# Optimization experiments

Hardware: AMD Instinct MI355X
Metric: run time of the kernel (lower is better)

Reference implementation:

```python
import jax, jax.numpy as jnp
import numpy as np

NUM_RBF = 16
RBF_D_MIN, RBF_D_MAX = 2.0, 22.0
CB_A, CB_B, CB_C = -0.58273431, 0.56802827, -0.54067466
TOP_K = 32
MAX_REL = 32
NPOS = 16
HID = 128
LN_EPS = 1e-5


def _gather_nodes(nodes, idx):
    # nodes: (B, L, D), idx: (B, L, K) -> (B, L, K, D)
    return jax.vmap(lambda n, i: n[i])(nodes, idx)


def _rbf_encode(D):
    mu = jnp.linspace(RBF_D_MIN, RBF_D_MAX, NUM_RBF, dtype=D.dtype)
    sigma = (RBF_D_MAX - RBF_D_MIN) / NUM_RBF
    return jnp.exp(-((D[..., None] - mu) ** 2) / (sigma ** 2))


def setup_inputs() -> dict:
    key = jax.random.key(0)
    ks = jax.random.split(key, 4)
    B, L = 2, 2048
    X = jax.random.normal(ks[0], (B, L, 4, 3), jnp.float32) * 10.0
    residue_mask = jnp.ones((B, L), jnp.float32)
    R_idx = jnp.arange(B * L, dtype=jnp.int32).reshape(B, L)
    chain_labels = jnp.zeros((B, L), jnp.int32)
    # learned params
    W_pos = jax.random.normal(ks[1], (NPOS, 2 * MAX_REL + 2), jnp.float32) * 0.05
    b_pos = jnp.zeros((NPOS,), jnp.float32)
    W_edge = jax.random.normal(ks[2], (HID, 25 * NUM_RBF + NPOS), jnp.float32) * 0.02
    ln_gamma = jnp.ones((HID,), jnp.float32)
    ln_beta = jnp.zeros((HID,), jnp.float32)
    return {"X": X, "residue_mask": residue_mask, "R_idx": R_idx,
            "chain_labels": chain_labels, "W_pos": W_pos, "b_pos": b_pos,
            "W_edge": W_edge, "ln_gamma": ln_gamma, "ln_beta": ln_beta}


def reference(X, residue_mask, R_idx, chain_labels, W_pos, b_pos, W_edge, ln_gamma, ln_beta):
    B, L = X.shape[0], X.shape[1]
    K = min(TOP_K, L)
    # virtual CB from backbone N, CA, C
    N, CA, C = X[..., 0, :], X[..., 1, :], X[..., 2, :]
    b = CA - N
    c = C - CA
    a = jnp.cross(b, c, axis=-1)
    CB = (CB_A * a + CB_B * b + CB_C * c + CA)[..., None, :]
    atoms_5 = jnp.concatenate([X, CB], axis=-2)  # (B, L, 5, 3)
    # kNN on CA coords with invalid residues pushed far away
    diff = CA[:, :, None, :] - CA[:, None, :, :]
    dist_sq = jnp.sum(diff * diff, axis=-1)  # (B, L, L)
    inv_mask = 1.0 - residue_mask
    dist_sq = dist_sq + inv_mask[:, None, :] * 1e6
    _, E_idx = jax.lax.top_k(-dist_sq, K)  # smallest-k indices, (B, L, K)
    # gather neighbor 5-atom coords and compute 25 pairwise distances
    Xf = atoms_5.reshape(B, L, 15)
    Xg = _gather_nodes(Xf, E_idx).reshape(B, L, K, 5, 3)
    d2 = jnp.sum((atoms_5[:, :, None, :, None, :] - Xg[:, :, :, None, :, :]) ** 2, axis=-1)
    D = jnp.sqrt(d2 + 1e-6)  # (B, L, K, 5, 5)
    rbf = _rbf_encode(D).reshape(B, L, K, 25 * NUM_RBF)
    # positional encodings (standard ProteinMPNN form)
    Rg = _gather_nodes(R_idx[..., None], E_idx)[..., 0]  # (B, L, K)
    Cg = _gather_nodes(chain_labels[..., None], E_idx)[..., 0]
    d_rel = Rg - R_idx[:, :, None]
    same_chain = (Cg == chain_labels[:, :, None])
    d_clip = jnp.clip(d_rel + MAX_REL, 0, 2 * MAX_REL)
    d_final = jnp.where(same_chain, d_clip, 2 * MAX_REL + 1)
    oh = jax.nn.one_hot(d_final, 2 * MAX_REL + 2, dtype=rbf.dtype)
    pos_enc = jnp.einsum('blkc,pc->blkp', oh, W_pos) + b_pos
    # edge embedding + layernorm
    edge_input = jnp.concatenate([pos_enc, rbf], axis=-1)  # (B, L, K, 416)
    h = jnp.einsum('blkf,hf->blkh', edge_input, W_edge)
    mean = jnp.mean(h, axis=-1, keepdims=True)
    var = jnp.var(h, axis=-1, keepdims=True)
    E = (h - mean) * jax.lax.rsqrt(var + LN_EPS) * ln_gamma + ln_beta
    return E_idx, E
```

## Files before the change

kernel.cpp:

```cpp
#include <hip/hip_runtime.h>
#include <hip/hip_bf16.h>

#define LEN   2048
#define KNB   32
#define HID   128

typedef unsigned long long ull;
typedef unsigned int uint32;
typedef __bf16 bf16x8 __attribute__((ext_vector_type(8)));
typedef float  f32x4  __attribute__((ext_vector_type(4)));

__global__ __launch_bounds__(256) void prep_kernel(
    const float* __restrict__ X, const float* __restrict__ mask,
    const float* __restrict__ W_edge,
    float4* __restrict__ CAm, __bf16* __restrict__ Wbf) {
    const int t = blockIdx.x * 256 + threadIdx.x;
    if (t < 2 * LEN) {
        const float* p = X + (size_t)t * 12;
        CAm[t] = make_float4(p[3], p[4], p[5],
                             __fmul_rn(__fsub_rn(1.0f, mask[t]), 1000000.0f));
    }
    Wbf[t] = (__bf16)W_edge[t];
}

__global__ __launch_bounds__(256) void topk_kernel(
    const float4* __restrict__ CAm, float* __restrict__ eidx_out) {
    const int row = blockIdx.x;
    const int b = row >> 11;
    const int i = row & (LEN - 1);
    const int tid = threadIdx.x;

    __shared__ int hist[512];
    __shared__ ull cand[LEN];
    __shared__ int candcnt;
    __shared__ int selB;

    const float4* C = CAm + (size_t)b * LEN;
    const float4 ci = C[i];

    uint32 d2b[8];
#pragma unroll
    for (int q = 0; q < 8; ++q) {
        const float4 cj = C[q * 256 + tid];
        float dx = __fsub_rn(ci.x, cj.x);
        float dy = __fsub_rn(ci.y, cj.y);
        float dz = __fsub_rn(ci.z, cj.z);
        float d2 = __fadd_rn(__fadd_rn(__fmul_rn(dx, dx), __fmul_rn(dy, dy)),
                             __fmul_rn(dz, dz));
        d2 = __fadd_rn(d2, cj.w);
        d2b[q] = __float_as_uint(d2);
    }

    hist[tid] = 0; hist[tid + 256] = 0;
    if (tid == 0) candcnt = 0;
    __syncthreads();
#pragma unroll
    for (int q = 0; q < 8; ++q) atomicAdd(&hist[d2b[q] >> 22], 1);
    __syncthreads();

    if (tid < 64) {
        int loc[8];
        int s = 0;
#pragma unroll
        for (int t = 0; t < 8; ++t) { loc[t] = hist[tid * 8 + t]; s += loc[t]; }
        int incl = s;
#pragma unroll
        for (int off = 1; off < 64; off <<= 1) {
            int o = __shfl_up(incl, off, 64);
            if (tid >= off) incl += o;
        }
        const int excl = incl - s;
        if (excl < KNB && incl >= KNB) {
            int c = excl;
#pragma unroll
            for (int t = 0; t < 8; ++t) {
                int c2 = c + loc[t];
                if (c < KNB && c2 >= KNB) selB = tid * 8 + t;
                c = c2;
            }
        }
    }
    __syncthreads();
    const uint32 B = (uint32)selB;

#pragma unroll
    for (int q = 0; q < 8; ++q) {
        if ((d2b[q] >> 22) <= B) {
            int p = atomicAdd(&candcnt, 1);
            cand[p] = (((ull)d2b[q]) << 32) | (uint32)(q * 256 + tid);
        }
    }
    __syncthreads();
    const int M = candcnt;

    for (int c = tid; c < M; c += 256) {
        const ull k = cand[c];
        int r = 0;
        for (int m = 0; m < M; ++m) r += (cand[m] < k);
        if (r < KNB)
            eidx_out[(size_t)row * KNB + r] = (float)(uint32)(k & 0xFFFFFFFFull);
    }
}

__device__ __forceinline__ void load_res_atoms(const float* __restrict__ p, float* dst) {
    const float Nx = p[0], Ny = p[1], Nz = p[2];
    const float Ax = p[3], Ay = p[4], Az = p[5];
    const float Cx = p[6], Cy = p[7], Cz = p[8];
    const float Ox = p[9], Oy = p[10], Oz = p[11];
    const float bx = Ax - Nx, by = Ay - Ny, bz = Az - Nz;
    const float cx = Cx - Ax, cy = Cy - Ay, cz = Cz - Az;
    const float axv = by * cz - bz * cy;
    const float ayv = bz * cx - bx * cz;
    const float azv = bx * cy - by * cx;
    dst[0] = Nx;  dst[1] = Ny;  dst[2] = Nz;
    dst[3] = Ax;  dst[4] = Ay;  dst[5] = Az;
    dst[6] = Cx;  dst[7] = Cy;  dst[8] = Cz;
    dst[9] = Ox;  dst[10] = Oy; dst[11] = Oz;
    dst[12] = -0.58273431f * axv + 0.56802827f * bx + -0.54067466f * cx + Ax;
    dst[13] = -0.58273431f * ayv + 0.56802827f * by + -0.54067466f * cy + Ay;
    dst[14] = -0.58273431f * azv + 0.56802827f * bz + -0.54067466f * cz + Az;
}

#define FSTRIDE 424

__global__ __launch_bounds__(512, 4) void edge_kernel(
    const float* __restrict__ X,
    const int* __restrict__ Ridx, const int* __restrict__ Chain,
    const float* __restrict__ W_pos, const float* __restrict__ b_pos,
    const __bf16* __restrict__ Wbf,
    const float* __restrict__ lng, const float* __restrict__ lnb,
    const float* __restrict__ eidx_f, float* __restrict__ outE) {
    const int tid = threadIdx.x;
    const int row0 = blockIdx.x * 8;
    const int b = row0 >> 11;
    const int i0 = row0 & (LEN - 1);

    __shared__ __align__(16) __bf16 featE[32 * FSTRIDE];
    __shared__ __align__(16) float hbuf[32 * 132];
    __shared__ float natoms8[8][32][17];
    __shared__ float iatoms8[8][16];
    __shared__ int jR8[8][32], jC8[8][32];

    const float* Xb = X + (size_t)b * LEN * 12;

    const int w = tid >> 6, l = tid & 63, lr = l & 15, lg = l >> 4;
    bf16x8 wreg[13];
    {
        const __bf16* wb = Wbf + (size_t)(w * 16 + lr) * 416 + lg * 8;
#pragma unroll
        for (int ks = 0; ks < 13; ++ks)
            wreg[ks] = *(const bf16x8*)(wb + ks * 32);
    }

    if (tid < 256) {
        const int r8 = tid >> 5, e = tid & 31;
        const int j = (int)eidx_f[(size_t)(row0 + r8) * KNB + e];
        jR8[r8][e] = Ridx[b * LEN + j];
        jC8[r8][e] = Chain[b * LEN + j];
        load_res_atoms(Xb + j * 12, &natoms8[r8][e][0]);
    } else if (tid < 264) {
        const int r8 = tid - 256;
        load_res_atoms(Xb + (size_t)(i0 + r8) * 12, &iatoms8[r8][0]);
    }
    __syncthreads();

    for (int r8 = 0; r8 < 8; ++r8) {
        const int row = row0 + r8;
        const int i = i0 + r8;
        const int Ri = Ridx[b * LEN + i];
        const int Ci = Chain[b * LEN + i];

        {
            const int e = tid >> 4, p = tid & 15;
            const int drel = jR8[r8][e] - Ri;
            const int same = (jC8[r8][e] == Ci);
            int dc = drel + 32;
            dc = dc < 0 ? 0 : (dc > 64 ? 64 : dc);
            const int df = same ? dc : 65;
            featE[e * FSTRIDE + p] = (__bf16)(W_pos[p * 66 + df] + b_pos[p]);
        }
#pragma unroll
        for (int it = 0; it < 2; ++it) {
            const int task = tid + it * 512;
            if (task < 800) {
                const int mn = task >> 5, e = task & 31;
                const int m = mn / 5, n = mn - m * 5;
                const float ax = iatoms8[r8][m * 3 + 0];
                const float ay = iatoms8[r8][m * 3 + 1];
                const float az = iatoms8[r8][m * 3 + 2];
                const float* na = &natoms8[r8][e][n * 3];
                const float dx = ax - na[0], dy = ay - na[1], dz = az - na[2];
                const float D = sqrtf(dx * dx + dy * dy + dz * dz + 1e-6f);
                bf16x8 v0, v1;
#pragma unroll
                for (int r = 0; r < 8; ++r) {
                    const float mu = (float)(2.0 + (double)r * (20.0 / 15.0));
                    const float t = D - mu;
                    v0[r] = (__bf16)__expf(-(t * t) * (1.0f / 1.5625f));
                }
#pragma unroll
                for (int r = 8; r < 16; ++r) {
                    const float mu = (float)(2.0 + (double)r * (20.0 / 15.0));
                    const float t = D - mu;
                    v1[r - 8] = (__bf16)__expf(-(t * t) * (1.0f / 1.5625f));
                }
                *(bf16x8*)(featE + e * FSTRIDE + 16 + mn * 16)     = v0;
                *(bf16x8*)(featE + e * FSTRIDE + 16 + mn * 16 + 8) = v1;
            }
        }
        __syncthreads();

        f32x4 acc0 = {0.f, 0.f, 0.f, 0.f}, acc1 = acc0;
        const __bf16* fb0 = featE + lr * FSTRIDE + lg * 8;
        const __bf16* fb1 = featE + (16 + lr) * FSTRIDE + lg * 8;
#pragma unroll
        for (int ks = 0; ks < 13; ++ks) {
            const bf16x8 a0 = *(const bf16x8*)(fb0 + ks * 32);
            const bf16x8 a1 = *(const bf16x8*)(fb1 + ks * 32);
            acc0 = __builtin_amdgcn_mfma_f32_16x16x32_bf16(a0, wreg[ks], acc0, 0, 0, 0);
            acc1 = __builtin_amdgcn_mfma_f32_16x16x32_bf16(a1, wreg[ks], acc1, 0, 0, 0);
        }
#pragma unroll
        for (int rr = 0; rr < 4; ++rr) {
            hbuf[(lg * 4 + rr) * 132 + w * 16 + lr]        = acc0[rr];
            hbuf[(16 + lg * 4 + rr) * 132 + w * 16 + lr]   = acc1[rr];
        }
        __syncthreads();

        const int g = tid >> 4, l2 = tid & 15;
        const float4* hb4 = (const float4*)(hbuf + g * 132 + l2 * 8);
        const float4 v0 = hb4[0], v1 = hb4[1];
        float s = v0.x + v0.y + v0.z + v0.w + v1.x + v1.y + v1.z + v1.w;
        float ssq = v0.x * v0.x + v0.y * v0.y + v0.z * v0.z + v0.w * v0.w
                  + v1.x * v1.x + v1.y * v1.y + v1.z * v1.z + v1.w * v1.w;
#pragma unroll
        for (int off = 1; off < 16; off <<= 1) {
            s += __shfl_xor(s, off, 64);
            ssq += __shfl_xor(ssq, off, 64);
        }
        const float mean = s * (1.0f / 128.0f);
        const float rstd = rsqrtf(ssq * (1.0f / 128.0f) - mean * mean + 1e-5f);

        float4* ob = (float4*)(outE + ((size_t)row * KNB + g) * HID + l2 * 8);
        const float4 g0 = *(const float4*)(lng + l2 * 8);
        const float4 g1 = *(const float4*)(lng + l2 * 8 + 4);
        const float4 b0 = *(const float4*)(lnb + l2 * 8);
        const float4 b1 = *(const float4*)(lnb + l2 * 8 + 4);
        float4 o0, o1;
        o0.x = (v0.x - mean) * rstd * g0.x + b0.x;
        o0.y = (v0.y - mean) * rstd * g0.y + b0.y;
        o0.z = (v0.z - mean) * rstd * g0.z + b0.z;
        o0.w = (v0.w - mean) * rstd * g0.w + b0.w;
        o1.x = (v1.x - mean) * rstd * g1.x + b1.x;
        o1.y = (v1.y - mean) * rstd * g1.y + b1.y;
        o1.z = (v1.z - mean) * rstd * g1.z + b1.z;
        o1.w = (v1.w - mean) * rstd * g1.w + b1.w;
        ob[0] = o0;
        ob[1] = o1;
    }
}

extern "C" void kernel_launch(void* const* d_in, const int* in_sizes, int n_in,
                              void* d_out, int out_size, void* d_ws, size_t ws_size,
                              hipStream_t stream) {
    const float* X      = (const float*)d_in[0];
    const float* mask   = (const float*)d_in[1];
    const int*   Ridx   = (const int*)d_in[2];
    const int*   Chain  = (const int*)d_in[3];
    const float* W_pos  = (const float*)d_in[4];
    const float* b_pos  = (const float*)d_in[5];
    const float* W_edge = (const float*)d_in[6];
    const float* lng    = (const float*)d_in[7];
    const float* lnb    = (const float*)d_in[8];

    float* out  = (float*)d_out;
    float* eidx = out;
    float* E    = out + (size_t)2 * LEN * KNB;

    float4* CAm = (float4*)d_ws;
    __bf16* Wbf = (__bf16*)((char*)d_ws + 2 * LEN * 16);

    const int nrow = 2 * LEN;
    prep_kernel<<<208, 256, 0, stream>>>(X, mask, W_edge, CAm, Wbf);
    topk_kernel<<<nrow, 256, 0, stream>>>(CAm, eidx);
    edge_kernel<<<nrow / 8, 512, 0, stream>>>(X, Ridx, Chain, W_pos, b_pos, Wbf,
                                              lng, lnb, eidx, E);
}
```

Before: 63.94 us.

## Compute LayerNorm stats in registers via shuffles and shared atomics, dropping hbuf

Removes the 17KB hbuf staging buffer. Each wave now reduces per-edge sum and sum-of-squares with shuffles and merges them across waves through shared-memory atomics into a double-buffered stats array, then normalizes straight from the MFMA accumulators. Feature building for the next row is moved after the output stores so one barrier per row is saved, and the occupancy hint rises from 4 to 6. The trade-off is stores of one float per lane at stride 128 (per edge row) instead of vectorized float4 writes, plus atomic contention on LDS.

```diff
diff --git a/kernel.cpp b/kernel.cpp
--- a/kernel.cpp
+++ b/kernel.cpp
@@ -123,7 +123,7 @@
 
 #define FSTRIDE 424
 
-__global__ __launch_bounds__(512, 4) void edge_kernel(
+__global__ __launch_bounds__(512, 6) void edge_kernel(
     const float* __restrict__ X,
     const int* __restrict__ Ridx, const int* __restrict__ Chain,
     const float* __restrict__ W_pos, const float* __restrict__ b_pos,
@@ -136,10 +136,10 @@
     const int i0 = row0 & (LEN - 1);
 
     __shared__ __align__(16) __bf16 featE[32 * FSTRIDE];
-    __shared__ __align__(16) float hbuf[32 * 132];
     __shared__ float natoms8[8][32][17];
     __shared__ float iatoms8[8][16];
     __shared__ int jR8[8][32], jC8[8][32];
+    __shared__ float sbuf[2][64];
 
     const float* Xb = X + (size_t)b * LEN * 12;
 
@@ -151,6 +151,8 @@
         for (int ks = 0; ks < 13; ++ks)
             wreg[ks] = *(const bf16x8*)(wb + ks * 32);
     }
+    const int chan = w * 16 + lr;
+    const float gam = lng[chan], bet = lnb[chan];
 
     if (tid < 256) {
         const int r8 = tid >> 5, e = tid & 31;
@@ -161,15 +163,15 @@
     } else if (tid < 264) {
         const int r8 = tid - 256;
         load_res_atoms(Xb + (size_t)(i0 + r8) * 12, &iatoms8[r8][0]);
-    }
-    __syncthreads();
-
-    for (int r8 = 0; r8 < 8; ++r8) {
-        const int row = row0 + r8;
-        const int i = i0 + r8;
-        const int Ri = Ridx[b * LEN + i];
-        const int Ci = Chain[b * LEN + i];
-
+    } else if (tid >= 384) {
+        sbuf[(tid - 384) >> 6][(tid - 384) & 63] = 0.0f;
+    }
+    __syncthreads();
+
+    {
+        const int r8 = 0;
+        const int Ri = Ridx[b * LEN + i0];
+        const int Ci = Chain[b * LEN + i0];
         {
             const int e = tid >> 4, p = tid & 15;
             const int drel = jR8[r8][e] - Ri;
@@ -208,55 +210,111 @@
                 *(bf16x8*)(featE + e * FSTRIDE + 16 + mn * 16 + 8) = v1;
             }
         }
+    }
+    __syncthreads();
+
+    for (int r8 = 0; r8 < 8; ++r8) {
+        const int row = row0 + r8;
+        const int par = r8 & 1;
+
+        if (tid < 64) sbuf[par ^ 1][tid] = 0.0f;
+
+        f32x4 acc0 = {0.f, 0.f, 0.f, 0.f}, acc1 = acc0;
+        {
+            const __bf16* fb0 = featE + lr * FSTRIDE + lg * 8;
+            const __bf16* fb1 = featE + (16 + lr) * FSTRIDE + lg * 8;
+#pragma unroll
+            for (int ks = 0; ks < 13; ++ks) {
+                const bf16x8 a0 = *(const bf16x8*)(fb0 + ks * 32);
+                const bf16x8 a1 = *(const bf16x8*)(fb1 + ks * 32);
+                acc0 = __builtin_amdgcn_mfma_f32_16x16x32_bf16(a0, wreg[ks], acc0, 0, 0, 0);
+                acc1 = __builtin_amdgcn_mfma_f32_16x16x32_bf16(a1, wreg[ks], acc1, 0, 0, 0);
+            }
+        }
+#pragma unroll
+        for (int rr = 0; rr < 4; ++rr) {
+            float s0 = acc0[rr], q0 = acc0[rr] * acc0[rr];
+            float s1 = acc1[rr], q1 = acc1[rr] * acc1[rr];
+#pragma unroll
+            for (int off = 1; off < 16; off <<= 1) {
+                s0 += __shfl_xor(s0, off, 64);
+                q0 += __shfl_xor(q0, off, 64);
+                s1 += __shfl_xor(s1, off, 64);
+                q1 += __shfl_xor(q1, off, 64);
+            }
+            if (lr == 0) {
+                const int e0 = lg * 4 + rr;
+                atomicAdd(&sbuf[par][e0 * 2 + 0], s0);
+                atomicAdd(&sbuf[par][e0 * 2 + 1], q0);
+                atomicAdd(&sbuf[par][(16 + e0) * 2 + 0], s1);
+                atomicAdd(&sbuf[par][(16 + e0) * 2 + 1], q1);
+            }
+        }
         __syncthreads();
 
-        f32x4 acc0 = {0.f, 0.f, 0.f, 0.f}, acc1 = acc0;
-        const __bf16* fb0 = featE + lr * FSTRIDE + lg * 8;
-        const __bf16* fb1 = featE + (16 + lr) * FSTRIDE + lg * 8;
-#pragma unroll
-        for (int ks = 0; ks < 13; ++ks) {
-            const bf16x8 a0 = *(const bf16x8*)(fb0 + ks * 32);
-            const bf16x8 a1 = *(const bf16x8*)(fb1 + ks * 32);
-            acc0 = __builtin_amdgcn_mfma_f32_16x16x32_bf16(a0, wreg[ks], acc0, 0, 0, 0);
-            acc1 = __builtin_amdgcn_mfma_f32_16x16x32_bf16(a1, wreg[ks], acc1, 0, 0, 0);
-        }
-#pragma unroll
-        for (int rr = 0; rr < 4; ++rr) {
-            hbuf[(lg * 4 + rr) * 132 + w * 16 + lr]        = acc0[rr];
-            hbuf[(16 + lg * 4 + rr) * 132 + w * 16 + lr]   = acc1[rr];
+        {
+            float* orow = outE + (size_t)(row * KNB) * HID + chan;
+#pragma unroll
+            for (int rr = 0; rr < 4; ++rr) {
+                const int e0 = lg * 4 + rr;
+                const float sS0 = sbuf[par][e0 * 2 + 0];
+                const float sQ0 = sbuf[par][e0 * 2 + 1];
+                const float mean0 = sS0 * (1.0f / 128.0f);
+                const float rstd0 = rsqrtf(sQ0 * (1.0f / 128.0f) - mean0 * mean0 + 1e-5f);
+                orow[(size_t)e0 * HID] = (acc0[rr] - mean0) * rstd0 * gam + bet;
+
+                const float sS1 = sbuf[par][(16 + e0) * 2 + 0];
+                const float sQ1 = sbuf[par][(16 + e0) * 2 + 1];
+                const float mean1 = sS1 * (1.0f / 128.0f);
+                const float rstd1 = rsqrtf(sQ1 * (1.0f / 128.0f) - mean1 * mean1 + 1e-5f);
+                orow[(size_t)(16 + e0) * HID] = (acc1[rr] - mean1) * rstd1 * gam + bet;
+            }
+        }
+        if (r8 < 7) {
+            const int rn = r8 + 1;
+            const int i = i0 + rn;
+            const int Ri = Ridx[b * LEN + i];
+            const int Ci = Chain[b * LEN + i];
+            {
+                const int e = tid >> 4, p = tid & 15;
+                const int drel = jR8[rn][e] - Ri;
+                const int same = (jC8[rn][e] == Ci);
+                int dc = drel + 32;
+                dc = dc < 0 ? 0 : (dc > 64 ? 64 : dc);
+                const int df = same ? dc : 65;
+                featE[e * FSTRIDE + p] = (__bf16)(W_pos[p * 66 + df] + b_pos[p]);
+            }
+#pragma unroll
+            for (int it = 0; it < 2; ++it) {
+                const int task = tid + it * 512;
+                if (task < 800) {
+                    const int mn = task >> 5, e = task & 31;
+                    const int m = mn / 5, n = mn - m * 5;
+                    const float ax = iatoms8[rn][m * 3 + 0];
+                    const float ay = iatoms8[rn][m * 3 + 1];
+                    const float az = iatoms8[rn][m * 3 + 2];
+                    const float* na = &natoms8[rn][e][n * 3];
+                    const float dx = ax - na[0], dy = ay - na[1], dz = az - na[2];
+                    const float D = sqrtf(dx * dx + dy * dy + dz * dz + 1e-6f);
+                    bf16x8 v0, v1;
+#pragma unroll
+                    for (int r = 0; r < 8; ++r) {
+                        const float mu = (float)(2.0 + (double)r * (20.0 / 15.0));
+                        const float t = D - mu;
+                        v0[r] = (__bf16)__expf(-(t * t) * (1.0f / 1.5625f));
+                    }
+#pragma unroll
+                    for (int r = 8; r < 16; ++r) {
+                        const float mu = (float)(2.0 + (double)r * (20.0 / 15.0));
+                        const float t = D - mu;
+                        v1[r - 8] = (__bf16)__expf(-(t * t) * (1.0f / 1.5625f));
+                    }
+                    *(bf16x8*)(featE + e * FSTRIDE + 16 + mn * 16)     = v0;
+                    *(bf16x8*)(featE + e * FSTRIDE + 16 + mn * 16 + 8) = v1;
+                }
+            }
         }
         __syncthreads();
-
-        const int g = tid >> 4, l2 = tid & 15;
-        const float4* hb4 = (const float4*)(hbuf + g * 132 + l2 * 8);
-        const float4 v0 = hb4[0], v1 = hb4[1];
-        float s = v0.x + v0.y + v0.z + v0.w + v1.x + v1.y + v1.z + v1.w;
-        float ssq = v0.x * v0.x + v0.y * v0.y + v0.z * v0.z + v0.w * v0.w
-                  + v1.x * v1.x + v1.y * v1.y + v1.z * v1.z + v1.w * v1.w;
-#pragma unroll
-        for (int off = 1; off < 16; off <<= 1) {
-            s += __shfl_xor(s, off, 64);
-            ssq += __shfl_xor(ssq, off, 64);
-        }
-        const float mean = s * (1.0f / 128.0f);
-        const float rstd = rsqrtf(ssq * (1.0f / 128.0f) - mean * mean + 1e-5f);
-
-        float4* ob = (float4*)(outE + ((size_t)row * KNB + g) * HID + l2 * 8);
-        const float4 g0 = *(const float4*)(lng + l2 * 8);
-        const float4 g1 = *(const float4*)(lng + l2 * 8 + 4);
-        const float4 b0 = *(const float4*)(lnb + l2 * 8);
-        const float4 b1 = *(const float4*)(lnb + l2 * 8 + 4);
-        float4 o0, o1;
-        o0.x = (v0.x - mean) * rstd * g0.x + b0.x;
-        o0.y = (v0.y - mean) * rstd * g0.y + b0.y;
-        o0.z = (v0.z - mean) * rstd * g0.z + b0.z;
-        o0.w = (v0.w - mean) * rstd * g0.w + b0.w;
-        o1.x = (v1.x - mean) * rstd * g1.x + b1.x;
-        o1.y = (v1.y - mean) * rstd * g1.y + b1.y;
-        o1.z = (v1.z - mean) * rstd * g1.z + b1.z;
-        o1.w = (v1.w - mean) * rstd * g1.w + b1.w;
-        ob[0] = o0;
-        ob[1] = o1;
     }
 }
 
```

New measurement: 116.5 us. 1.82x slower.

## Pipeline edge kernel rows: prefetch next row's neighbors and overlap feature build

Applied to the files above, without the earlier changes.

The edge kernel now handles 4 rows per block instead of 8, doubling the grid. Neighbor gathering for the next row is issued right after the current row's MFMA, using double-buffered shared arrays. The next row's features are built right after the layernorm store, which removes one barrier per row. The risks are more blocks each reloading the W registers, and a single-warp gather that sits on the critical path between rows.

```diff
diff --git a/kernel.cpp b/kernel.cpp
--- a/kernel.cpp
+++ b/kernel.cpp
@@ -123,6 +123,52 @@
 
 #define FSTRIDE 424
 
+__device__ __forceinline__ void compute_features(
+    int tid, int Ri, int Ci,
+    const float* __restrict__ W_pos, const float* __restrict__ b_pos,
+    const int* jR, const int* jC,
+    const float (*natoms)[17], const float* iatoms,
+    __bf16* featE) {
+    {
+        const int e = tid >> 4, p = tid & 15;
+        const int drel = jR[e] - Ri;
+        const int same = (jC[e] == Ci);
+        int dc = drel + 32;
+        dc = dc < 0 ? 0 : (dc > 64 ? 64 : dc);
+        const int df = same ? dc : 65;
+        featE[e * FSTRIDE + p] = (__bf16)(W_pos[p * 66 + df] + b_pos[p]);
+    }
+#pragma unroll
+    for (int it = 0; it < 2; ++it) {
+        const int task = tid + it * 512;
+        if (task < 800) {
+            const int mn = task >> 5, e = task & 31;
+            const int m = mn / 5, n = mn - m * 5;
+            const float ax = iatoms[m * 3 + 0];
+            const float ay = iatoms[m * 3 + 1];
+            const float az = iatoms[m * 3 + 2];
+            const float* na = &natoms[e][n * 3];
+            const float dx = ax - na[0], dy = ay - na[1], dz = az - na[2];
+            const float D = sqrtf(dx * dx + dy * dy + dz * dz + 1e-6f);
+            bf16x8 v0, v1;
+#pragma unroll
+            for (int r = 0; r < 8; ++r) {
+                const float mu = (float)(2.0 + (double)r * (20.0 / 15.0));
+                const float t = D - mu;
+                v0[r] = (__bf16)__expf(-(t * t) * (1.0f / 1.5625f));
+            }
+#pragma unroll
+            for (int r = 8; r < 16; ++r) {
+                const float mu = (float)(2.0 + (double)r * (20.0 / 15.0));
+                const float t = D - mu;
+                v1[r - 8] = (__bf16)__expf(-(t * t) * (1.0f / 1.5625f));
+            }
+            *(bf16x8*)(featE + e * FSTRIDE + 16 + mn * 16)     = v0;
+            *(bf16x8*)(featE + e * FSTRIDE + 16 + mn * 16 + 8) = v1;
+        }
+    }
+}
+
 __global__ __launch_bounds__(512, 4) void edge_kernel(
     const float* __restrict__ X,
     const int* __restrict__ Ridx, const int* __restrict__ Chain,
@@ -131,15 +177,15 @@
     const float* __restrict__ lng, const float* __restrict__ lnb,
     const float* __restrict__ eidx_f, float* __restrict__ outE) {
     const int tid = threadIdx.x;
-    const int row0 = blockIdx.x * 8;
+    const int row0 = blockIdx.x * 4;
     const int b = row0 >> 11;
     const int i0 = row0 & (LEN - 1);
 
     __shared__ __align__(16) __bf16 featE[32 * FSTRIDE];
     __shared__ __align__(16) float hbuf[32 * 132];
-    __shared__ float natoms8[8][32][17];
-    __shared__ float iatoms8[8][16];
-    __shared__ int jR8[8][32], jC8[8][32];
+    __shared__ float natoms[2][32][17];
+    __shared__ float iatoms[2][16];
+    __shared__ int jR[2][32], jC[2][32];
 
     const float* Xb = X + (size_t)b * LEN * 12;
 
@@ -152,111 +198,91 @@
             wreg[ks] = *(const bf16x8*)(wb + ks * 32);
     }
 
-    if (tid < 256) {
-        const int r8 = tid >> 5, e = tid & 31;
-        const int j = (int)eidx_f[(size_t)(row0 + r8) * KNB + e];
-        jR8[r8][e] = Ridx[b * LEN + j];
-        jC8[r8][e] = Chain[b * LEN + j];
-        load_res_atoms(Xb + j * 12, &natoms8[r8][e][0]);
-    } else if (tid < 264) {
-        const int r8 = tid - 256;
-        load_res_atoms(Xb + (size_t)(i0 + r8) * 12, &iatoms8[r8][0]);
-    }
-    __syncthreads();
-
-    for (int r8 = 0; r8 < 8; ++r8) {
-        const int row = row0 + r8;
-        const int i = i0 + r8;
-        const int Ri = Ridx[b * LEN + i];
-        const int Ci = Chain[b * LEN + i];
-
+    if (tid < 32) {
+        const int j = (int)eidx_f[(size_t)row0 * KNB + tid];
+        jR[0][tid] = Ridx[b * LEN + j];
+        jC[0][tid] = Chain[b * LEN + j];
+        load_res_atoms(Xb + j * 12, &natoms[0][tid][0]);
+    } else if (tid == 32) {
+        load_res_atoms(Xb + (size_t)i0 * 12, &iatoms[0][0]);
+    }
+    __syncthreads();
+    compute_features(tid, Ridx[b * LEN + i0], Chain[b * LEN + i0],
+                     W_pos, b_pos, jR[0], jC[0], natoms[0], iatoms[0], featE);
+    __syncthreads();
+
+    for (int r = 0; r < 4; ++r) {
+        const int row = row0 + r;
+        const int nb = (r + 1) & 1;
+
+        f32x4 acc0 = {0.f, 0.f, 0.f, 0.f}, acc1 = acc0;
         {
-            const int e = tid >> 4, p = tid & 15;
-            const int drel = jR8[r8][e] - Ri;
-            const int same = (jC8[r8][e] == Ci);
-            int dc = drel + 32;
-            dc = dc < 0 ? 0 : (dc > 64 ? 64 : dc);
-            const int df = same ? dc : 65;
-            featE[e * FSTRIDE + p] = (__bf16)(W_pos[p * 66 + df] + b_pos[p]);
-        }
-#pragma unroll
-        for (int it = 0; it < 2; ++it) {
-            const int task = tid + it * 512;
-            if (task < 800) {
-                const int mn = task >> 5, e = task & 31;
-                const int m = mn / 5, n = mn - m * 5;
-                const float ax = iatoms8[r8][m * 3 + 0];
-                const float ay = iatoms8[r8][m * 3 + 1];
-                const float az = iatoms8[r8][m * 3 + 2];
-                const float* na = &natoms8[r8][e][n * 3];
-                const float dx = ax - na[0], dy = ay - na[1], dz = az - na[2];
-                const float D = sqrtf(dx * dx + dy * dy + dz * dz + 1e-6f);
-                bf16x8 v0, v1;
-#pragma unroll
-                for (int r = 0; r < 8; ++r) {
-                    const float mu = (float)(2.0 + (double)r * (20.0 / 15.0));
-                    const float t = D - mu;
-                    v0[r] = (__bf16)__expf(-(t * t) * (1.0f / 1.5625f));
-                }
-#pragma unroll
-                for (int r = 8; r < 16; ++r) {
-                    const float mu = (float)(2.0 + (double)r * (20.0 / 15.0));
-                    const float t = D - mu;
-                    v1[r - 8] = (__bf16)__expf(-(t * t) * (1.0f / 1.5625f));
-                }
-                *(bf16x8*)(featE + e * FSTRIDE + 16 + mn * 16)     = v0;
-                *(bf16x8*)(featE + e * FSTRIDE + 16 + mn * 16 + 8) = v1;
-            }
+            const __bf16* fb0 = featE + lr * FSTRIDE + lg * 8;
+            const __bf16* fb1 = featE + (16 + lr) * FSTRIDE + lg * 8;
+#pragma unroll
+            for (int ks = 0; ks < 13; ++ks) {
+                const bf16x8 a0 = *(const bf16x8*)(fb0 + ks * 32);
+                const bf16x8 a1 = *(const bf16x8*)(fb1 + ks * 32);
+                acc0 = __builtin_amdgcn_mfma_f32_16x16x32_bf16(a0, wreg[ks], acc0, 0, 0, 0);
+                acc1 = __builtin_amdgcn_mfma_f32_16x16x32_bf16(a1, wreg[ks], acc1, 0, 0, 0);
+            }
+        }
+        if (r < 3) {
+            if (tid < 32) {
+                const int j = (int)eidx_f[(size_t)(row + 1) * KNB + tid];
+                jR[nb][tid] = Ridx[b * LEN + j];
+                jC[nb][tid] = Chain[b * LEN + j];
+                load_res_atoms(Xb + j * 12, &natoms[nb][tid][0]);
+            } else if (tid == 32) {
+                load_res_atoms(Xb + (size_t)(i0 + r + 1) * 12, &iatoms[nb][0]);
+            }
+        }
+#pragma unroll
+        for (int rr = 0; rr < 4; ++rr) {
+            hbuf[(lg * 4 + rr) * 132 + w * 16 + lr]      = acc0[rr];
+            hbuf[(16 + lg * 4 + rr) * 132 + w * 16 + lr] = acc1[rr];
         }
         __syncthreads();
 
-        f32x4 acc0 = {0.f, 0.f, 0.f, 0.f}, acc1 = acc0;
-        const __bf16* fb0 = featE + lr * FSTRIDE + lg * 8;
-        const __bf16* fb1 = featE + (16 + lr) * FSTRIDE + lg * 8;
-#pragma unroll
-        for (int ks = 0; ks < 13; ++ks) {
-            const bf16x8 a0 = *(const bf16x8*)(fb0 + ks * 32);
-            const bf16x8 a1 = *(const bf16x8*)(fb1 + ks * 32);
-            acc0 = __builtin_amdgcn_mfma_f32_16x16x32_bf16(a0, wreg[ks], acc0, 0, 0, 0);
-            acc1 = __builtin_amdgcn_mfma_f32_16x16x32_bf16(a1, wreg[ks], acc1, 0, 0, 0);
-        }
-#pragma unroll
-        for (int rr = 0; rr < 4; ++rr) {
-            hbuf[(lg * 4 + rr) * 132 + w * 16 + lr]        = acc0[rr];
-            hbuf[(16 + lg * 4 + rr) * 132 + w * 16 + lr]   = acc1[rr];
+        {
+            const int g = tid >> 4, l2 = tid & 15;
+            const float4* hb4 = (const float4*)(hbuf + g * 132 + l2 * 8);
+            const float4 v0 = hb4[0], v1 = hb4[1];
+            float s = v0.x + v0.y + v0.z + v0.w + v1.x + v1.y + v1.z + v1.w;
+            float ssq = v0.x * v0.x + v0.y * v0.y + v0.z * v0.z + v0.w * v0.w
+                      + v1.x * v1.x + v1.y * v1.y + v1.z * v1.z + v1.w * v1.w;
+#pragma unroll
+            for (int off = 1; off < 16; off <<= 1) {
+                s += __shfl_xor(s, off, 64);
+                ssq += __shfl_xor(ssq, off, 64);
+            }
+            const float mean = s * (1.0f / 128.0f);
+            const float rstd = rsqrtf(ssq * (1.0f / 128.0f) - mean * mean + 1e-5f);
+
+            float4* ob = (float4*)(outE + ((size_t)row * KNB + g) * HID + l2 * 8);
+            const float4 g0 = *(const float4*)(lng + l2 * 8);
+            const float4 g1 = *(const float4*)(lng + l2 * 8 + 4);
+            const float4 b0 = *(const float4*)(lnb + l2 * 8);
+            const float4 b1 = *(const float4*)(lnb + l2 * 8 + 4);
+            float4 o0, o1;
+            o0.x = (v0.x - mean) * rstd * g0.x + b0.x;
+            o0.y = (v0.y - mean) * rstd * g0.y + b0.y;
+            o0.z = (v0.z - mean) * rstd * g0.z + b0.z;
+            o0.w = (v0.w - mean) * rstd * g0.w + b0.w;
+            o1.x = (v1.x - mean) * rstd * g1.x + b1.x;
+            o1.y = (v1.y - mean) * rstd * g1.y + b1.y;
+            o1.z = (v1.z - mean) * rstd * g1.z + b1.z;
+            o1.w = (v1.w - mean) * rstd * g1.w + b1.w;
+            ob[0] = o0;
+            ob[1] = o1;
+        }
+        if (r < 3) {
+            const int i = i0 + r + 1;
+            compute_features(tid, Ridx[b * LEN + i], Chain[b * LEN + i],
+                             W_pos, b_pos, jR[nb], jC[nb], natoms[nb], iatoms[nb],
+                             featE);
         }
         __syncthreads();
-
-        const int g = tid >> 4, l2 = tid & 15;
-        const float4* hb4 = (const float4*)(hbuf + g * 132 + l2 * 8);
-        const float4 v0 = hb4[0], v1 = hb4[1];
-        float s = v0.x + v0.y + v0.z + v0.w + v1.x + v1.y + v1.z + v1.w;
-        float ssq = v0.x * v0.x + v0.y * v0.y + v0.z * v0.z + v0.w * v0.w
-                  + v1.x * v1.x + v1.y * v1.y + v1.z * v1.z + v1.w * v1.w;
-#pragma unroll
-        for (int off = 1; off < 16; off <<= 1) {
-            s += __shfl_xor(s, off, 64);
-            ssq += __shfl_xor(ssq, off, 64);
-        }
-        const float mean = s * (1.0f / 128.0f);
-        const float rstd = rsqrtf(ssq * (1.0f / 128.0f) - mean * mean + 1e-5f);
-
-        float4* ob = (float4*)(outE + ((size_t)row * KNB + g) * HID + l2 * 8);
-        const float4 g0 = *(const float4*)(lng + l2 * 8);
-        const float4 g1 = *(const float4*)(lng + l2 * 8 + 4);
-        const float4 b0 = *(const float4*)(lnb + l2 * 8);
-        const float4 b1 = *(const float4*)(lnb + l2 * 8 + 4);
-        float4 o0, o1;
-        o0.x = (v0.x - mean) * rstd * g0.x + b0.x;
-        o0.y = (v0.y - mean) * rstd * g0.y + b0.y;
-        o0.z = (v0.z - mean) * rstd * g0.z + b0.z;
-        o0.w = (v0.w - mean) * rstd * g0.w + b0.w;
-        o1.x = (v1.x - mean) * rstd * g1.x + b1.x;
-        o1.y = (v1.y - mean) * rstd * g1.y + b1.y;
-        o1.z = (v1.z - mean) * rstd * g1.z + b1.z;
-        o1.w = (v1.w - mean) * rstd * g1.w + b1.w;
-        ob[0] = o0;
-        ob[1] = o1;
     }
 }
 
@@ -283,6 +309,6 @@
     const int nrow = 2 * LEN;
     prep_kernel<<<208, 256, 0, stream>>>(X, mask, W_edge, CAm, Wbf);
     topk_kernel<<<nrow, 256, 0, stream>>>(CAm, eidx);
-    edge_kernel<<<nrow / 8, 512, 0, stream>>>(X, Ridx, Chain, W_pos, b_pos, Wbf,
+    edge_kernel<<<nrow / 4, 512, 0, stream>>>(X, Ridx, Chain, W_pos, b_pos, Wbf,
                                               lng, lnb, eidx, E);
 }
```

New measurement: 71.70 us. +12.1%, slower.
